# Performance work log

Measured on AMD Instinct MI355X. Metric: run time of the kernel, lower is better.

Reference implementation:

```python
import jax, jax.numpy as jnp
import numpy as np

H = 2048          # hidden_size
NH = 16           # num query heads
NKV = 8           # num kv heads
HD = 128          # head_dim
T = 4096          # tokens (single causal prefill sequence)
THETA = 1000000.0
EPS = 1e-6
QS = NH * HD
KVS = NKV * HD
SCALE = HD ** -0.5


def setup_inputs() -> dict:
    key = jax.random.key(0)
    k0, k1, k2 = jax.random.split(key, 3)
    return {
        "positions": jnp.arange(T, dtype=jnp.int32),
        "hidden_states": jax.random.normal(k0, (T, H), jnp.float32),
        "w_qkv": jax.random.normal(k1, (H, QS + 2 * KVS), jnp.float32) * 0.02,
        "w_o": jax.random.normal(k2, (QS, H), jnp.float32) * 0.02,
        "q_norm_w": jnp.ones((HD,), jnp.float32),
        "k_norm_w": jnp.ones((HD,), jnp.float32),
    }


def _rmsnorm(x, w):
    # per-head RMSNorm over last dim (head_dim)
    return x * jax.lax.rsqrt(jnp.mean(x * x, axis=-1, keepdims=True) + EPS) * w


def _rope(x, cos, sin):
    # neox-style rotate-half RoPE; x: [T, nheads, HD], cos/sin: [T, 1, HD/2]
    x1, x2 = jnp.split(x, 2, axis=-1)
    return jnp.concatenate([x1 * cos - x2 * sin, x2 * cos + x1 * sin], axis=-1)


def reference(positions, hidden_states, w_qkv, w_o, q_norm_w, k_norm_w):
    # fused QKV projection then split
    qkv = hidden_states @ w_qkv                      # [T, QS+2*KVS]
    q, k, v = jnp.split(qkv, [QS, QS + KVS], axis=-1)
    q = _rmsnorm(q.reshape(T, NH, HD), q_norm_w)     # per-head QK RMSNorm
    k = _rmsnorm(k.reshape(T, NKV, HD), k_norm_w)
    v = v.reshape(T, NKV, HD)

    # RoPE over full head_dim
    inv_freq = 1.0 / (THETA ** (jnp.arange(0, HD, 2, dtype=jnp.float32) / HD))
    ang = positions.astype(jnp.float32)[:, None] * inv_freq  # [T, HD/2]
    cos = jnp.cos(ang)[:, None, :]
    sin = jnp.sin(ang)[:, None, :]
    q = _rope(q, cos, sin)
    k = _rope(k, cos, sin)

    # causal GQA attention (prefill path of RadixAttention)
    G = NH // NKV
    q4 = q.reshape(T, NKV, G, HD) * SCALE
    scores = jnp.einsum('tkgd,skd->kgts', q4, k)     # [NKV, G, T, T]
    causal = jnp.tril(jnp.ones((T, T), dtype=bool))
    scores = jnp.where(causal, scores, jnp.float32(-1e30))
    probs = jax.nn.softmax(scores, axis=-1)
    out = jnp.einsum('kgts,skd->tkgd', probs, v).reshape(T, QS)
    return out @ w_o
```

## Files before the change

kernel.cpp:

```cpp
#include <hip/hip_runtime.h>
#include <hip/hip_bf16.h>
#include <math.h>

#define T_TOK 4096
#define H_DIM 2048
#define NH 16
#define NKV 8
#define HD 128
#define QS (NH * HD)
#define KVS (NKV * HD)
#define QKV_W (QS + 2*KVS)
#define QSCALE (0.08838834764831845f * 1.4426950408889634f)
#define EPS 1e-6f

typedef short short8 __attribute__((ext_vector_type(8)));
typedef short short4v __attribute__((ext_vector_type(4)));
typedef float floatx4 __attribute__((ext_vector_type(4)));

#if __has_builtin(__builtin_amdgcn_exp2f)
#define EXP2(x) __builtin_amdgcn_exp2f(x)
#else
#define EXP2(x) exp2f(x)
#endif

__device__ __forceinline__ unsigned short f2bf(float f) {
    unsigned int u = __float_as_uint(f);
    unsigned int r = (u + 0x7FFFu + ((u >> 16) & 1u)) >> 16;
    return (unsigned short)r;
}
__device__ __forceinline__ float bf2f(unsigned short u) {
    unsigned int v = ((unsigned int)u) << 16;
    return __uint_as_float(v);
}
__device__ __forceinline__ unsigned int pk2(float a, float b) {
    union { __hip_bfloat162 h; unsigned int u; } c;
    c.h = __float22bfloat162_rn(make_float2(a, b));
    return c.u;
}

__device__ __forceinline__ void gload_lds16(const unsigned short* g, unsigned short* l) {
    __builtin_amdgcn_global_load_lds(
        (const __attribute__((address_space(1))) unsigned int*)(const void*)g,
        (__attribute__((address_space(3))) unsigned int*)(void*)l, 16, 0, 0);
}

__global__ __launch_bounds__(256) void cvt_bf16(const float* __restrict__ in,
                                                unsigned short* __restrict__ out) {
    int idx = (blockIdx.x * 256 + threadIdx.x) * 8;
    float4 v0 = *(const float4*)&in[idx];
    float4 v1 = *(const float4*)&in[idx + 4];
    short8 t;
    t[0] = (short)f2bf(v0.x); t[1] = (short)f2bf(v0.y);
    t[2] = (short)f2bf(v0.z); t[3] = (short)f2bf(v0.w);
    t[4] = (short)f2bf(v1.x); t[5] = (short)f2bf(v1.y);
    t[6] = (short)f2bf(v1.z); t[7] = (short)f2bf(v1.w);
    *(short8*)&out[idx] = t;
}

__global__ __launch_bounds__(256) void cvt_transpose(const float* __restrict__ in,
                                                     unsigned short* __restrict__ out,
                                                     int K, int N) {
    __shared__ __align__(16) unsigned short t[64][72];
    const int tid = threadIdx.x;
    const int n0 = blockIdx.x * 64, k0 = blockIdx.y * 64;
    const int r = tid >> 4, c4 = (tid & 15) * 4;
    #pragma unroll
    for (int i = 0; i < 4; ++i) {
        int kk = r + 16 * i;
        float4 v = *(const float4*)&in[(size_t)(k0 + kk) * N + n0 + c4];
        t[c4 + 0][kk] = f2bf(v.x); t[c4 + 1][kk] = f2bf(v.y);
        t[c4 + 2][kk] = f2bf(v.z); t[c4 + 3][kk] = f2bf(v.w);
    }
    __syncthreads();
    const int n = tid >> 2, c8 = (tid & 3) * 16;
    short8 a = *(const short8*)&t[n][c8];
    short8 b = *(const short8*)&t[n][c8 + 8];
    *(short8*)&out[(size_t)(n0 + n) * K + k0 + c8] = a;
    *(short8*)&out[(size_t)(n0 + n) * K + k0 + c8 + 8] = b;
}

template<bool C_BF16>
__global__ __launch_bounds__(256) void gemm_bt(const unsigned short* __restrict__ A, int lda,
                                               const unsigned short* __restrict__ Bt, int ldb,
                                               void* __restrict__ Cptr, int ldc, int K) {
    __shared__ __align__(16) unsigned short As[128 * 32];
    __shared__ __align__(16) unsigned short Bs[128 * 32];
    const int tid = threadIdx.x;
    const int wave = tid >> 6, lane = tid & 63;
    const int quad = lane >> 4, l16 = lane & 15;
    const int wm = wave >> 1, wn = wave & 1;
    const int bm = blockIdx.y * 128, bn = blockIdx.x * 128;

    floatx4 acc[4][4] = {};
    for (int k0 = 0; k0 < K; k0 += 32) {
        #pragma unroll
        for (int i = 0; i < 2; ++i) {
            int c = wave * 128 + i * 64 + lane;
            int row = c >> 2, off = (c & 3) * 8;
            gload_lds16(A  + (size_t)(bm + row) * lda + k0 + off, As + (size_t)(wave * 128 + i * 64) * 8);
            gload_lds16(Bt + (size_t)(bn + row) * ldb + k0 + off, Bs + (size_t)(wave * 128 + i * 64) * 8);
        }
        __syncthreads();
        short8 a[4], b[4];
        #pragma unroll
        for (int mi = 0; mi < 4; ++mi)
            a[mi] = *(const short8*)&As[(wm * 64 + mi * 16 + l16) * 32 + quad * 8];
        #pragma unroll
        for (int ni = 0; ni < 4; ++ni)
            b[ni] = *(const short8*)&Bs[(wn * 64 + ni * 16 + l16) * 32 + quad * 8];
        #pragma unroll
        for (int mi = 0; mi < 4; ++mi)
            #pragma unroll
            for (int ni = 0; ni < 4; ++ni)
                acc[mi][ni] = __builtin_amdgcn_mfma_f32_16x16x32_bf16(a[mi], b[ni], acc[mi][ni], 0, 0, 0);
        __syncthreads();
    }
    #pragma unroll
    for (int mi = 0; mi < 4; ++mi)
        #pragma unroll
        for (int ni = 0; ni < 4; ++ni)
            #pragma unroll
            for (int r = 0; r < 4; ++r) {
                int row = bm + wm * 64 + mi * 16 + quad * 4 + r;
                int col = bn + wn * 64 + ni * 16 + l16;
                if (C_BF16)
                    ((unsigned short*)Cptr)[(size_t)row * ldc + col] = f2bf(acc[mi][ni][r]);
                else
                    ((float*)Cptr)[(size_t)row * ldc + col] = acc[mi][ni][r];
            }
}

__global__ __launch_bounds__(256) void rms_rope_bf16(unsigned short* __restrict__ qkv,
                                                     const int* __restrict__ positions,
                                                     const float* __restrict__ qw,
                                                     const float* __restrict__ kw) {
    const int t = blockIdx.x;
    const int wave = threadIdx.x >> 6;
    const int lane = threadIdx.x & 63;
    const float pos = (float)positions[t];
    unsigned short* row = qkv + (size_t)t * QKV_W;
    const float inv_freq = powf(1000000.0f, -(float)lane / 64.0f);
    float sv, cv;
    sincosf(pos * inv_freq, &sv, &cv);
    for (int h = wave; h < NH + NKV; h += 4) {
        unsigned short* x = row + h * HD;
        const float* w = (h < NH) ? qw : kw;
        const float hs = (h < NH) ? QSCALE : 1.0f;
        float x1 = bf2f(x[lane]);
        float x2 = bf2f(x[lane + 64]);
        float ss = x1 * x1 + x2 * x2;
        #pragma unroll
        for (int off = 32; off > 0; off >>= 1) ss += __shfl_xor(ss, off, 64);
        float r = rsqrtf(ss * (1.0f / 128.0f) + EPS) * hs;
        float n1 = x1 * r * w[lane];
        float n2 = x2 * r * w[lane + 64];
        x[lane]      = f2bf(n1 * cv - n2 * sv);
        x[lane + 64] = f2bf(n2 * cv + n1 * sv);
    }
}

__global__ __launch_bounds__(256) void kv_pack(const unsigned short* __restrict__ qkv,
                                               unsigned short* __restrict__ Kp,
                                               unsigned short* __restrict__ Vp) {
    const int tile = blockIdx.x, kvh = blockIdx.y, tid = threadIdx.x;
    const int t0 = tile * 128;
    const size_t tb = (size_t)(kvh * 32 + tile) * 16384;
    #pragma unroll
    for (int i = 0; i < 8; ++i) {
        int cid = i * 256 + tid;
        int s = cid >> 4, c = cid & 15;
        short8 v = *(const short8*)&qkv[(size_t)(t0 + s) * QKV_W + QS + kvh * HD + c * 8];
        *(short8*)&Kp[tb + (s * 16 + (c ^ (s & 7))) * 8] = v;
    }
    __shared__ __align__(16) unsigned short Lt[128 * 136];
    #pragma unroll
    for (int i = 0; i < 8; ++i) {
        int cid = i * 256 + tid;
        int s = cid >> 4, c = cid & 15;
        short8 v = *(const short8*)&qkv[(size_t)(t0 + s) * QKV_W + QS + KVS + kvh * HD + c * 8];
        #pragma unroll
        for (int e = 0; e < 8; ++e)
            Lt[(c * 8 + e) * 136 + s] = (unsigned short)v[e];
    }
    __syncthreads();
    #pragma unroll
    for (int i = 0; i < 8; ++i) {
        int cid = i * 256 + tid;
        int d = cid >> 4, cs = cid & 15;
        short8 v = *(const short8*)&Lt[d * 136 + cs * 8];
        short8 w;
        if ((d >> 3) & 1) {
            #pragma unroll
            for (int e = 0; e < 8; ++e) w[e] = v[e ^ 4];
        } else w = v;
        *(short8*)&Vp[tb + (d * 16 + (cs ^ (d & 7))) * 8] = w;
    }
}

__global__ __launch_bounds__(256, 2) void attn_mfma(unsigned short* __restrict__ qkv,
                                                    const unsigned short* __restrict__ Kp,
                                                    const unsigned short* __restrict__ Vp) {
    __shared__ __align__(16) unsigned short Ks[128 * 128];
    __shared__ __align__(16) unsigned short Vs[128 * 128];
    const int bx = blockIdx.x;
    const int h = bx & 15, kvh = h >> 1;
    const int g = bx >> 4;
    const int qt = (g < 16) ? (31 - g) : (g - 16);
    const int tid = threadIdx.x;
    const int wave = tid >> 6, lane = tid & 63;
    const int quad = lane >> 4, l16 = lane & 15;
    const int t0 = qt * 128;
    const int wrow0 = t0 + wave * 32;
    const int swz = l16 & 7;
    const int hsel = (l16 >> 3) & 1;
    const int vhalf = ((quad & 1) ^ hsel) * 4;
    const int q2 = quad >> 1;

    short8 qf[2][4];
    #pragma unroll
    for (int rt = 0; rt < 2; ++rt)
        #pragma unroll
        for (int ks = 0; ks < 4; ++ks) {
            int rowg = t0 + wave * 32 + rt * 16 + l16;
            qf[rt][ks] = *(const short8*)&qkv[(size_t)rowg * QKV_W + h * HD + ks * 32 + quad * 8];
        }

    float l_s[2] = {};
    floatx4 oacc[2][8] = {};

    for (int st = 0; st <= qt; ++st) {
        const int s0 = st * 128;
        const unsigned short* kb = Kp + (size_t)(kvh * 32 + st) * 16384;
        const unsigned short* vb = Vp + (size_t)(kvh * 32 + st) * 16384;
        #pragma unroll
        for (int i = 0; i < 8; ++i) {
            int ch = i * 256 + tid;
            gload_lds16(kb + (size_t)ch * 8, Ks + (i * 256 + wave * 64) * 8);
        }
        #pragma unroll
        for (int i = 0; i < 8; ++i) {
            int ch = i * 256 + tid;
            gload_lds16(vb + (size_t)ch * 8, Vs + (i * 256 + wave * 64) * 8);
        }
        __syncthreads();

        const bool diag = (st == qt);
        #pragma unroll
        for (int ct = 0; ct < 8; ++ct) {
            const int smin = s0 + ct * 16;
            if (diag && smin > wrow0 + 31) continue;
            floatx4 sacc[2] = {};
            #pragma unroll
            for (int ks = 0; ks < 4; ++ks) {
                short8 kfr = *(const short8*)&Ks[(ct * 16 + l16) * 128 + ((ks * 4 + quad) ^ swz) * 8];
                sacc[0] = __builtin_amdgcn_mfma_f32_16x16x32_bf16(kfr, qf[0][ks], sacc[0], 0, 0, 0);
                sacc[1] = __builtin_amdgcn_mfma_f32_16x16x32_bf16(kfr, qf[1][ks], sacc[1], 0, 0, 0);
            }
            short4v pp[2];
            #pragma unroll
            for (int rt = 0; rt < 2; ++rt) {
                const int tg = wrow0 + rt * 16 + l16;
                float p[4];
                float lsum = 0.0f;
                #pragma unroll
                for (int r = 0; r < 4; ++r) {
                    float s = sacc[rt][r];
                    if (diag && (smin + quad * 4 + r > tg)) s = -1e30f;
                    p[r] = EXP2(s);
                    lsum += p[r];
                }
                l_s[rt] += lsum;
                union { short4v s4; unsigned int u[2]; } pk;
                pk.u[0] = pk2(p[0], p[1]);
                pk.u[1] = pk2(p[2], p[3]);
                pp[rt] = pk.s4;
            }
            const int vc = (((ct * 2 + q2) ^ swz)) * 8 + vhalf;
#if __has_builtin(__builtin_amdgcn_mfma_f32_16x16x16bf16_1k)
            #pragma unroll
            for (int dct = 0; dct < 8; ++dct) {
                short4v bfr = *(const short4v*)&Vs[(dct * 16 + l16) * 128 + vc];
                oacc[0][dct] = __builtin_amdgcn_mfma_f32_16x16x16bf16_1k(pp[0], bfr, oacc[0][dct], 0, 0, 0);
                oacc[1][dct] = __builtin_amdgcn_mfma_f32_16x16x16bf16_1k(pp[1], bfr, oacc[1][dct], 0, 0, 0);
            }
#else
            #pragma unroll
            for (int dct = 0; dct < 8; ++dct) {
                union { short8 s8; short4v s4[2]; } b;
                b.s4[0] = *(const short4v*)&Vs[(dct * 16 + l16) * 128 + vc];
                b.s4[1] = short4v{0, 0, 0, 0};
                #pragma unroll
                for (int rt = 0; rt < 2; ++rt) {
                    union { short8 s8; short4v s4[2]; } a;
                    a.s4[0] = pp[rt];
                    a.s4[1] = short4v{0, 0, 0, 0};
                    oacc[rt][dct] = __builtin_amdgcn_mfma_f32_16x16x32_bf16(a.s8, b.s8, oacc[rt][dct], 0, 0, 0);
                }
            }
#endif
        }
        __syncthreads();
    }

    float lred[2];
    #pragma unroll
    for (int rt = 0; rt < 2; ++rt) {
        float l = l_s[rt];
        l += __shfl_xor(l, 16, 64);
        l += __shfl_xor(l, 32, 64);
        lred[rt] = l;
    }
    #pragma unroll
    for (int rt = 0; rt < 2; ++rt)
        #pragma unroll
        for (int r = 0; r < 4; ++r) {
            float l = __shfl(lred[rt], quad * 4 + r, 64);
            float linv = 1.0f / l;
            int rowg = t0 + wave * 32 + rt * 16 + quad * 4 + r;
            #pragma unroll
            for (int dct = 0; dct < 8; ++dct)
                qkv[(size_t)rowg * QKV_W + h * HD + dct * 16 + l16] = f2bf(oacc[rt][dct][r] * linv);
        }
}

extern "C" void kernel_launch(void* const* d_in, const int* in_sizes, int n_in,
                              void* d_out, int out_size, void* d_ws, size_t ws_size,
                              hipStream_t stream) {
    const int*   positions = (const int*)d_in[0];
    const float* hidden    = (const float*)d_in[1];
    const float* w_qkv     = (const float*)d_in[2];
    const float* w_o       = (const float*)d_in[3];
    const float* q_norm_w  = (const float*)d_in[4];
    const float* k_norm_w  = (const float*)d_in[5];
    float* out = (float*)d_out;

    unsigned short* qkvb   = (unsigned short*)d_ws;
    unsigned short* h_bf   = (unsigned short*)((char*)d_ws + ((size_t)32 << 20));
    unsigned short* Kp     = (unsigned short*)((char*)d_ws + ((size_t)32 << 20));
    unsigned short* Vp     = (unsigned short*)((char*)d_ws + ((size_t)40 << 20));
    unsigned short* wqkv_t = (unsigned short*)((char*)d_ws + ((size_t)48 << 20));
    unsigned short* wo_t   = (unsigned short*)((char*)d_ws + ((size_t)48 << 20));

    cvt_bf16<<<(T_TOK * H_DIM) / (256 * 8), 256, 0, stream>>>(hidden, h_bf);
    cvt_transpose<<<dim3(QKV_W / 64, H_DIM / 64), 256, 0, stream>>>(w_qkv, wqkv_t, H_DIM, QKV_W);
    gemm_bt<true><<<dim3(QKV_W / 128, T_TOK / 128), 256, 0, stream>>>(
        h_bf, H_DIM, wqkv_t, H_DIM, qkvb, QKV_W, H_DIM);
    rms_rope_bf16<<<T_TOK, 256, 0, stream>>>(qkvb, positions, q_norm_w, k_norm_w);
    kv_pack<<<dim3(T_TOK / 128, NKV), 256, 0, stream>>>(qkvb, Kp, Vp);
    cvt_transpose<<<dim3(H_DIM / 64, QS / 64), 256, 0, stream>>>(w_o, wo_t, QS, H_DIM);
    attn_mfma<<<512, 256, 0, stream>>>(qkvb, Kp, Vp);
    gemm_bt<false><<<dim3(H_DIM / 128, T_TOK / 128), 256, 0, stream>>>(
        qkvb, QKV_W, wo_t, QS, out, H_DIM, QS);
}
```

Measured before the change: 410.2 us.

## Replace GEMM with 256x256-tile multistage pipelined kernel using swizzled LDS

Replaces the 128x128 single-buffered bf16 MFMA GEMM with a 256x256-tile, 512-thread kernel. It streams K through a four-slot LDS ring using direct global-to-LDS loads, with manual vmcnt waits and barriers. The kernel also XOR-swizzles LDS columns to reduce bank conflicts, remaps block indices for L2 locality, and raises wave priority around the MFMA bursts. It is meant to hide global-load latency and improve operand reuse in both projection GEMMs. The cost is fewer blocks (256 and 128) on a large-CU device, plus heavier register and LDS use.

```diff
diff --git a/kernel.cpp b/kernel.cpp
--- a/kernel.cpp
+++ b/kernel.cpp
@@ -80,48 +80,103 @@
 }
 
 template<bool C_BF16>
-__global__ __launch_bounds__(256) void gemm_bt(const unsigned short* __restrict__ A, int lda,
-                                               const unsigned short* __restrict__ Bt, int ldb,
-                                               void* __restrict__ Cptr, int ldc, int K) {
-    __shared__ __align__(16) unsigned short As[128 * 32];
-    __shared__ __align__(16) unsigned short Bs[128 * 32];
-    const int tid = threadIdx.x;
+__global__ __launch_bounds__(512, 2) void gemm256(const unsigned short* __restrict__ A, int lda,
+                                                  const unsigned short* __restrict__ Bt, int ldb,
+                                                  void* __restrict__ Cptr, int ldc, int K, int nbx) {
+    __shared__ __align__(16) unsigned short lds[4 * 16384];
+    const int tid  = threadIdx.x;
     const int wave = tid >> 6, lane = tid & 63;
     const int quad = lane >> 4, l16 = lane & 15;
-    const int wm = wave >> 1, wn = wave & 1;
-    const int bm = blockIdx.y * 128, bn = blockIdx.x * 128;
-
-    floatx4 acc[4][4] = {};
-    for (int k0 = 0; k0 < K; k0 += 32) {
-        #pragma unroll
-        for (int i = 0; i < 2; ++i) {
-            int c = wave * 128 + i * 64 + lane;
-            int row = c >> 2, off = (c & 3) * 8;
-            gload_lds16(A  + (size_t)(bm + row) * lda + k0 + off, As + (size_t)(wave * 128 + i * 64) * 8);
-            gload_lds16(Bt + (size_t)(bn + row) * ldb + k0 + off, Bs + (size_t)(wave * 128 + i * 64) * 8);
-        }
-        __syncthreads();
-        short8 a[4], b[4];
-        #pragma unroll
-        for (int mi = 0; mi < 4; ++mi)
-            a[mi] = *(const short8*)&As[(wm * 64 + mi * 16 + l16) * 32 + quad * 8];
+    const int wm = wave >> 2, wn = wave & 3;
+
+    const int cpx = gridDim.x >> 3;
+    const int swz = (blockIdx.x & 7) * cpx + (blockIdx.x >> 3);
+    const int by = swz / nbx, bx = swz % nbx;
+    const int bm = by * 256, bn = bx * 256;
+
+    const int ch0 = wave * 64 + lane;
+    const int ch1 = 512 + ch0;
+    const int ar0 = ch0 >> 2, ac0 = ((ch0 & 3) ^ (ar0 & 3)) * 8;
+    const int ar1 = ch1 >> 2, ac1 = ((ch1 & 3) ^ (ar1 & 3)) * 8;
+    const unsigned short* a0 = A  + (size_t)(bm + ar0) * lda + ac0;
+    const unsigned short* a1 = A  + (size_t)(bm + ar1) * lda + ac1;
+    const unsigned short* b0 = Bt + (size_t)(bn + ar0) * ldb + ac0;
+    const unsigned short* b1 = Bt + (size_t)(bn + ar1) * ldb + ac1;
+    const unsigned du0 = (unsigned)(wave * 64) * 8;
+    const unsigned du1 = (unsigned)(512 + wave * 64) * 8;
+
+    auto stage = [&](int kofs, int sb) {
+        gload_lds16(a0 + kofs, &lds[sb + du0]);
+        gload_lds16(a1 + kofs, &lds[sb + du1]);
+        gload_lds16(b0 + kofs, &lds[sb + 8192 + du0]);
+        gload_lds16(b1 + kofs, &lds[sb + 8192 + du1]);
+    };
+
+    floatx4 acc[8][4] = {};
+    const int arow = wm * 128 + l16;
+    const int brow = wn * 64 + l16;
+    const int sslot = (quad ^ (l16 & 3)) * 8;
+
+    auto compute = [&](int cbo) {
+        short8 bfr[4];
         #pragma unroll
         for (int ni = 0; ni < 4; ++ni)
-            b[ni] = *(const short8*)&Bs[(wn * 64 + ni * 16 + l16) * 32 + quad * 8];
-        #pragma unroll
-        for (int mi = 0; mi < 4; ++mi)
+            bfr[ni] = *(const short8*)&lds[cbo + 8192 + (brow + ni * 16) * 32 + sslot];
+        __builtin_amdgcn_s_setprio(1);
+        #pragma unroll
+        for (int mi = 0; mi < 8; ++mi) {
+            short8 afr = *(const short8*)&lds[cbo + (arow + mi * 16) * 32 + sslot];
             #pragma unroll
             for (int ni = 0; ni < 4; ++ni)
-                acc[mi][ni] = __builtin_amdgcn_mfma_f32_16x16x32_bf16(a[mi], b[ni], acc[mi][ni], 0, 0, 0);
-        __syncthreads();
-    }
-    #pragma unroll
-    for (int mi = 0; mi < 4; ++mi)
+                acc[mi][ni] = __builtin_amdgcn_mfma_f32_16x16x32_bf16(afr, bfr[ni], acc[mi][ni], 0, 0, 0);
+        }
+        __builtin_amdgcn_s_setprio(0);
+    };
+
+    const int NT = K >> 5;
+    stage(0,  0);
+    stage(32, 16384);
+    stage(64, 32768);
+
+    int cb = 0;
+    for (int t = 0; t < NT - 3; ++t) {
+        stage((t + 3) * 32, (cb + 3 * 16384) & 65535);
+        asm volatile("s_waitcnt vmcnt(12)" ::: "memory");
+        __builtin_amdgcn_s_barrier();
+        asm volatile("" ::: "memory");
+        compute(cb);
+        asm volatile("" ::: "memory");
+        __builtin_amdgcn_s_barrier();
+        cb = (cb + 16384) & 65535;
+    }
+    asm volatile("s_waitcnt vmcnt(8)" ::: "memory");
+    __builtin_amdgcn_s_barrier();
+    asm volatile("" ::: "memory");
+    compute(cb);
+    asm volatile("" ::: "memory");
+    __builtin_amdgcn_s_barrier();
+    cb = (cb + 16384) & 65535;
+
+    asm volatile("s_waitcnt vmcnt(4)" ::: "memory");
+    __builtin_amdgcn_s_barrier();
+    asm volatile("" ::: "memory");
+    compute(cb);
+    asm volatile("" ::: "memory");
+    __builtin_amdgcn_s_barrier();
+    cb = (cb + 16384) & 65535;
+
+    asm volatile("s_waitcnt vmcnt(0)" ::: "memory");
+    __builtin_amdgcn_s_barrier();
+    asm volatile("" ::: "memory");
+    compute(cb);
+
+    #pragma unroll
+    for (int mi = 0; mi < 8; ++mi)
         #pragma unroll
         for (int ni = 0; ni < 4; ++ni)
             #pragma unroll
             for (int r = 0; r < 4; ++r) {
-                int row = bm + wm * 64 + mi * 16 + quad * 4 + r;
+                int row = bm + wm * 128 + mi * 16 + quad * 4 + r;
                 int col = bn + wn * 64 + ni * 16 + l16;
                 if (C_BF16)
                     ((unsigned short*)Cptr)[(size_t)row * ldc + col] = f2bf(acc[mi][ni][r]);
@@ -343,12 +398,12 @@
 
     cvt_bf16<<<(T_TOK * H_DIM) / (256 * 8), 256, 0, stream>>>(hidden, h_bf);
     cvt_transpose<<<dim3(QKV_W / 64, H_DIM / 64), 256, 0, stream>>>(w_qkv, wqkv_t, H_DIM, QKV_W);
-    gemm_bt<true><<<dim3(QKV_W / 128, T_TOK / 128), 256, 0, stream>>>(
-        h_bf, H_DIM, wqkv_t, H_DIM, qkvb, QKV_W, H_DIM);
+    gemm256<true><<<dim3(256), 512, 0, stream>>>(
+        h_bf, H_DIM, wqkv_t, H_DIM, qkvb, QKV_W, H_DIM, QKV_W / 256);
     rms_rope_bf16<<<T_TOK, 256, 0, stream>>>(qkvb, positions, q_norm_w, k_norm_w);
     kv_pack<<<dim3(T_TOK / 128, NKV), 256, 0, stream>>>(qkvb, Kp, Vp);
     cvt_transpose<<<dim3(H_DIM / 64, QS / 64), 256, 0, stream>>>(w_o, wo_t, QS, H_DIM);
     attn_mfma<<<512, 256, 0, stream>>>(qkvb, Kp, Vp);
-    gemm_bt<false><<<dim3(H_DIM / 128, T_TOK / 128), 256, 0, stream>>>(
-        qkvb, QKV_W, wo_t, QS, out, H_DIM, QS);
-}
+    gemm256<false><<<dim3(128), 512, 0, stream>>>(
+        qkvb, QKV_W, wo_t, QS, out, H_DIM, QS, H_DIM / 256);
+}
```

After: 384.5 us. 6.2% less time.

## Add 8-wave 256x256 pipelined GEMM for QKV projection with XCD-aware block swizzle

Applied to the files above, without the earlier changes.

Adds a new 512-thread GEMM kernel that uses 256x256 output tiles, double-buffered direct-to-LDS global loads staged in quarters, and interleaves LDS fragment reads with MFMA groups under barriers and priority bumps. The QKV projection now uses it, with blocks remapped so neighbouring tiles land on the same XCD. The change also replaces powf with exp2f for the RoPE frequencies and rotates the V transpose LDS write order to reduce bank conflicts. The aim is better MFMA utilisation and overlap of memory with compute in the largest GEMM, at the cost of high register pressure (128 accumulators per lane) and a fixed grid of 256 blocks.

```diff
diff --git a/kernel.cpp b/kernel.cpp
--- a/kernel.cpp
+++ b/kernel.cpp
@@ -130,6 +130,116 @@
             }
 }
 
+template<bool C_BF16>
+__global__ __launch_bounds__(512, 2) void gemm8p(const unsigned short* __restrict__ A, int lda,
+                                                 const unsigned short* __restrict__ Bt, int ldb,
+                                                 void* __restrict__ Cptr, int ldc, int K, int nbx) {
+    __shared__ __align__(16) unsigned short lds[2 * 32768];
+    const int tid  = threadIdx.x;
+    const int wave = tid >> 6, lane = tid & 63;
+    const int quad = lane >> 4, l16 = lane & 15;
+    const int wm = wave >> 2, wn = wave & 3;
+
+    const int cpx = gridDim.x >> 3;
+    const int swzb = (blockIdx.x & 7) * cpx + (blockIdx.x >> 3);
+    const int by = swzb / nbx, bx = swzb % nbx;
+    const int bm = by * 256, bn = bx * 256;
+
+    const int ch0 = wave * 64 + lane, ch1 = 512 + ch0;
+    const int r0 = ch0 >> 3, gc0 = ((ch0 & 7) ^ (r0 & 7)) * 8;
+    const int r1 = ch1 >> 3, gc1 = ((ch1 & 7) ^ (r1 & 7)) * 8;
+    const unsigned du0 = (unsigned)(wave * 64) * 8;
+    const unsigned du1 = (unsigned)(512 + wave * 64) * 8;
+
+    auto stage = [&](int kt, int hf, int buf) {
+        const int panel = hf & 1, rhalf = (hf >> 1) * 128;
+        const unsigned short* P = panel ? Bt : A;
+        const int bp = panel ? bn : bm;
+        const int ld = panel ? ldb : lda;
+        unsigned short* dst = &lds[buf * 32768 + panel * 16384 + rhalf * 64];
+        gload_lds16(P + (size_t)(bp + rhalf + r0) * ld + kt * 64 + gc0, dst + du0);
+        gload_lds16(P + (size_t)(bp + rhalf + r1) * ld + kt * 64 + gc1, dst + du1);
+    };
+
+    floatx4 acc[8][4] = {};
+    const int arowb = wm * 128 + l16;
+    const int browb = wn * 64 + l16;
+    const int sw = l16 & 7;
+
+    short8 bfr[4], afr[4];
+    auto rdB = [&](int cur, int kk) {
+        const int sl = ((kk * 4 + quad) ^ sw) * 8;
+        #pragma unroll
+        for (int ni = 0; ni < 4; ++ni)
+            bfr[ni] = *(const short8*)&lds[cur * 32768 + 16384 + (browb + ni * 16) * 64 + sl];
+    };
+    auto rdA = [&](int cur, int mh, int kk) {
+        const int sl = ((kk * 4 + quad) ^ sw) * 8;
+        #pragma unroll
+        for (int mi = 0; mi < 4; ++mi)
+            afr[mi] = *(const short8*)&lds[cur * 32768 + (arowb + (mh * 4 + mi) * 16) * 64 + sl];
+    };
+    auto mfma16 = [&](int mh) {
+        asm volatile("s_waitcnt lgkmcnt(0)" ::: "memory");
+        __builtin_amdgcn_s_setprio(1);
+        #pragma unroll
+        for (int mi = 0; mi < 4; ++mi)
+            #pragma unroll
+            for (int ni = 0; ni < 4; ++ni)
+                acc[mh * 4 + mi][ni] =
+                    __builtin_amdgcn_mfma_f32_16x16x32_bf16(afr[mi], bfr[ni], acc[mh * 4 + mi][ni], 0, 0, 0);
+        __builtin_amdgcn_s_setprio(0);
+    };
+
+    const int NT = K >> 6;
+    stage(0, 0, 0); stage(0, 1, 0); stage(0, 2, 0); stage(0, 3, 0);
+
+    int cur = 0;
+    for (int kt = 0; kt < NT; ++kt) {
+        const bool last = (kt == NT - 1);
+        if (!last) {
+            stage(kt + 1, 0, cur ^ 1);
+            asm volatile("s_waitcnt vmcnt(2)" ::: "memory");
+        } else {
+            asm volatile("s_waitcnt vmcnt(0)" ::: "memory");
+        }
+        __builtin_amdgcn_s_barrier();
+        rdB(cur, 0); rdA(cur, 0, 0);
+        mfma16(0);
+        __builtin_amdgcn_s_barrier();
+        rdA(cur, 1, 0);
+        if (!last) stage(kt + 1, 1, cur ^ 1);
+        __builtin_amdgcn_s_barrier();
+        mfma16(1);
+        __builtin_amdgcn_s_barrier();
+        rdB(cur, 1); rdA(cur, 0, 1);
+        if (!last) stage(kt + 1, 2, cur ^ 1);
+        __builtin_amdgcn_s_barrier();
+        mfma16(0);
+        __builtin_amdgcn_s_barrier();
+        rdA(cur, 1, 1);
+        if (!last) stage(kt + 1, 3, cur ^ 1);
+        __builtin_amdgcn_s_barrier();
+        mfma16(1);
+        __builtin_amdgcn_s_barrier();
+        cur ^= 1;
+    }
+
+    #pragma unroll
+    for (int mi = 0; mi < 8; ++mi)
+        #pragma unroll
+        for (int ni = 0; ni < 4; ++ni)
+            #pragma unroll
+            for (int r = 0; r < 4; ++r) {
+                int row = bm + wm * 128 + mi * 16 + quad * 4 + r;
+                int col = bn + wn * 64 + ni * 16 + l16;
+                if (C_BF16)
+                    ((unsigned short*)Cptr)[(size_t)row * ldc + col] = f2bf(acc[mi][ni][r]);
+                else
+                    ((float*)Cptr)[(size_t)row * ldc + col] = acc[mi][ni][r];
+            }
+}
+
 __global__ __launch_bounds__(256) void rms_rope_bf16(unsigned short* __restrict__ qkv,
                                                      const int* __restrict__ positions,
                                                      const float* __restrict__ qw,
@@ -139,7 +249,7 @@
     const int lane = threadIdx.x & 63;
     const float pos = (float)positions[t];
     unsigned short* row = qkv + (size_t)t * QKV_W;
-    const float inv_freq = powf(1000000.0f, -(float)lane / 64.0f);
+    const float inv_freq = exp2f(-(float)lane * (19.931568569324174f / 64.0f));
     float sv, cv;
     sincosf(pos * inv_freq, &sv, &cv);
     for (int h = wave; h < NH + NKV; h += 4) {
@@ -179,8 +289,10 @@
         int s = cid >> 4, c = cid & 15;
         short8 v = *(const short8*)&qkv[(size_t)(t0 + s) * QKV_W + QS + KVS + kvh * HD + c * 8];
         #pragma unroll
-        for (int e = 0; e < 8; ++e)
-            Lt[(c * 8 + e) * 136 + s] = (unsigned short)v[e];
+        for (int e = 0; e < 8; ++e) {
+            int ee = (e + c) & 7;
+            Lt[(c * 8 + ee) * 136 + s] = (unsigned short)v[ee];
+        }
     }
     __syncthreads();
     #pragma unroll
@@ -343,8 +455,8 @@
 
     cvt_bf16<<<(T_TOK * H_DIM) / (256 * 8), 256, 0, stream>>>(hidden, h_bf);
     cvt_transpose<<<dim3(QKV_W / 64, H_DIM / 64), 256, 0, stream>>>(w_qkv, wqkv_t, H_DIM, QKV_W);
-    gemm_bt<true><<<dim3(QKV_W / 128, T_TOK / 128), 256, 0, stream>>>(
-        h_bf, H_DIM, wqkv_t, H_DIM, qkvb, QKV_W, H_DIM);
+    gemm8p<true><<<dim3(256), 512, 0, stream>>>(
+        h_bf, H_DIM, wqkv_t, H_DIM, qkvb, QKV_W, H_DIM, QKV_W / 256);
     rms_rope_bf16<<<T_TOK, 256, 0, stream>>>(qkvb, positions, q_norm_w, k_norm_w);
     kv_pack<<<dim3(T_TOK / 128, NKV), 256, 0, stream>>>(qkvb, Kp, Vp);
     cvt_transpose<<<dim3(H_DIM / 64, QS / 64), 256, 0, stream>>>(w_o, wo_t, QS, H_DIM);
```

Measured after the change: 369.6 us. 1.11x faster.

## Replace GEMM with double-buffered 256-row tile kernel using swizzled LDS and block remap

Applied to the files above, without the earlier changes.

Replaces the 128x128 single-buffered bf16 GEMM with a 512-thread kernel that uses 256xBN tiles and a K-step of 64. It double-buffers LDS with direct global-to-LDS loads, XOR-swizzles columns to avoid bank conflicts, and remaps block IDs for better L2 locality. It also raises MFMA priority during compute. Smaller tweaks replace powf with exp2f for the RoPE frequencies and rotate the write order in the V transpose to reduce LDS bank conflicts. The larger tiles raise register and LDS pressure per block, which can lower occupancy.

```diff
diff --git a/kernel.cpp b/kernel.cpp
--- a/kernel.cpp
+++ b/kernel.cpp
@@ -79,50 +79,96 @@
     *(short8*)&out[(size_t)(n0 + n) * K + k0 + c8 + 8] = b;
 }
 
-template<bool C_BF16>
-__global__ __launch_bounds__(256) void gemm_bt(const unsigned short* __restrict__ A, int lda,
-                                               const unsigned short* __restrict__ Bt, int ldb,
-                                               void* __restrict__ Cptr, int ldc, int K) {
-    __shared__ __align__(16) unsigned short As[128 * 32];
-    __shared__ __align__(16) unsigned short Bs[128 * 32];
-    const int tid = threadIdx.x;
+template<bool C_BF16, int BN>
+__global__ __launch_bounds__(512, 2) void gemm8p(const unsigned short* __restrict__ A, int lda,
+                                                 const unsigned short* __restrict__ Bt, int ldb,
+                                                 void* __restrict__ Cptr, int ldc, int K, int nbx) {
+    constexpr int LDSTILE = 16384 + BN * 64;
+    constexpr int NFRAG = BN / 64;
+    __shared__ __align__(16) unsigned short lds[2 * LDSTILE];
+    const int tid  = threadIdx.x;
     const int wave = tid >> 6, lane = tid & 63;
     const int quad = lane >> 4, l16 = lane & 15;
-    const int wm = wave >> 1, wn = wave & 1;
-    const int bm = blockIdx.y * 128, bn = blockIdx.x * 128;
-
-    floatx4 acc[4][4] = {};
-    for (int k0 = 0; k0 < K; k0 += 32) {
-        #pragma unroll
-        for (int i = 0; i < 2; ++i) {
-            int c = wave * 128 + i * 64 + lane;
-            int row = c >> 2, off = (c & 3) * 8;
-            gload_lds16(A  + (size_t)(bm + row) * lda + k0 + off, As + (size_t)(wave * 128 + i * 64) * 8);
-            gload_lds16(Bt + (size_t)(bn + row) * ldb + k0 + off, Bs + (size_t)(wave * 128 + i * 64) * 8);
-        }
-        __syncthreads();
-        short8 a[4], b[4];
-        #pragma unroll
-        for (int mi = 0; mi < 4; ++mi)
-            a[mi] = *(const short8*)&As[(wm * 64 + mi * 16 + l16) * 32 + quad * 8];
-        #pragma unroll
-        for (int ni = 0; ni < 4; ++ni)
-            b[ni] = *(const short8*)&Bs[(wn * 64 + ni * 16 + l16) * 32 + quad * 8];
-        #pragma unroll
-        for (int mi = 0; mi < 4; ++mi)
-            #pragma unroll
-            for (int ni = 0; ni < 4; ++ni)
-                acc[mi][ni] = __builtin_amdgcn_mfma_f32_16x16x32_bf16(a[mi], b[ni], acc[mi][ni], 0, 0, 0);
-        __syncthreads();
-    }
-    #pragma unroll
-    for (int mi = 0; mi < 4; ++mi)
-        #pragma unroll
-        for (int ni = 0; ni < 4; ++ni)
+    const int wm = wave >> 2, wn = wave & 3;
+
+    const int cpx = gridDim.x >> 3;
+    const int swzb = (blockIdx.x & 7) * cpx + (blockIdx.x >> 3);
+    const int by = swzb / nbx, bx = swzb % nbx;
+    const int bm = by * 256, bn = bx * BN;
+
+    const int ch0 = wave * 64 + lane, ch1 = 512 + ch0;
+    const int r0 = ch0 >> 3, gc0 = ((ch0 & 7) ^ (r0 & 7)) * 8;
+    const int r1 = ch1 >> 3, gc1 = ((ch1 & 7) ^ (r1 & 7)) * 8;
+    const unsigned du0 = (unsigned)(wave * 64) * 8;
+    const unsigned du1 = (unsigned)(512 + wave * 64) * 8;
+
+    auto stageP = [&](const unsigned short* P, int bp, int ld,
+                      unsigned short* dstbase, int rhalf, int kt) {
+        unsigned short* dst = dstbase + rhalf * 64;
+        gload_lds16(P + (size_t)(bp + rhalf + r0) * ld + kt * 64 + gc0, dst + du0);
+        gload_lds16(P + (size_t)(bp + rhalf + r1) * ld + kt * 64 + gc1, dst + du1);
+    };
+    auto stage = [&](int kt, int buf) {
+        unsigned short* ab = &lds[buf * LDSTILE];
+        unsigned short* bb = ab + 16384;
+        stageP(A, bm, lda, ab, 0, kt);
+        stageP(A, bm, lda, ab, 128, kt);
+        stageP(Bt, bn, ldb, bb, 0, kt);
+        if (BN == 256) stageP(Bt, bn, ldb, bb, 128, kt);
+    };
+
+    floatx4 acc[8][NFRAG] = {};
+    const int arowb = wm * 128 + l16;
+    const int browb = wn * (BN / 4) + l16;
+    const int sw = l16 & 7;
+
+    auto compute = [&](int buf) {
+        const unsigned short* ab = &lds[buf * LDSTILE];
+        const unsigned short* bb = ab + 16384;
+        __builtin_amdgcn_s_setprio(1);
+        #pragma unroll
+        for (int kk = 0; kk < 2; ++kk) {
+            const int sl = ((kk * 4 + quad) ^ sw) * 8;
+            short8 bfr[NFRAG];
+            #pragma unroll
+            for (int ni = 0; ni < NFRAG; ++ni)
+                bfr[ni] = *(const short8*)&bb[(browb + ni * 16) * 64 + sl];
+            #pragma unroll
+            for (int mh = 0; mh < 2; ++mh) {
+                short8 afr[4];
+                #pragma unroll
+                for (int mi = 0; mi < 4; ++mi)
+                    afr[mi] = *(const short8*)&ab[(arowb + (mh * 4 + mi) * 16) * 64 + sl];
+                #pragma unroll
+                for (int mi = 0; mi < 4; ++mi)
+                    #pragma unroll
+                    for (int ni = 0; ni < NFRAG; ++ni)
+                        acc[mh * 4 + mi][ni] =
+                            __builtin_amdgcn_mfma_f32_16x16x32_bf16(afr[mi], bfr[ni], acc[mh * 4 + mi][ni], 0, 0, 0);
+            }
+        }
+        __builtin_amdgcn_s_setprio(0);
+    };
+
+    const int NT = K >> 6;
+    stage(0, 0);
+    int cur = 0;
+    for (int kt = 0; kt < NT; ++kt) {
+        asm volatile("s_waitcnt vmcnt(0)" ::: "memory");
+        __builtin_amdgcn_s_barrier();
+        if (kt + 1 < NT) stage(kt + 1, cur ^ 1);
+        compute(cur);
+        cur ^= 1;
+    }
+
+    #pragma unroll
+    for (int mi = 0; mi < 8; ++mi)
+        #pragma unroll
+        for (int ni = 0; ni < NFRAG; ++ni)
             #pragma unroll
             for (int r = 0; r < 4; ++r) {
-                int row = bm + wm * 64 + mi * 16 + quad * 4 + r;
-                int col = bn + wn * 64 + ni * 16 + l16;
+                int row = bm + wm * 128 + mi * 16 + quad * 4 + r;
+                int col = bn + wn * (BN / 4) + ni * 16 + l16;
                 if (C_BF16)
                     ((unsigned short*)Cptr)[(size_t)row * ldc + col] = f2bf(acc[mi][ni][r]);
                 else
@@ -139,7 +185,7 @@
     const int lane = threadIdx.x & 63;
     const float pos = (float)positions[t];
     unsigned short* row = qkv + (size_t)t * QKV_W;
-    const float inv_freq = powf(1000000.0f, -(float)lane / 64.0f);
+    const float inv_freq = exp2f(-(float)lane * (19.931568569324174f / 64.0f));
     float sv, cv;
     sincosf(pos * inv_freq, &sv, &cv);
     for (int h = wave; h < NH + NKV; h += 4) {
@@ -179,8 +225,10 @@
         int s = cid >> 4, c = cid & 15;
         short8 v = *(const short8*)&qkv[(size_t)(t0 + s) * QKV_W + QS + KVS + kvh * HD + c * 8];
         #pragma unroll
-        for (int e = 0; e < 8; ++e)
-            Lt[(c * 8 + e) * 136 + s] = (unsigned short)v[e];
+        for (int e = 0; e < 8; ++e) {
+            int ee = (e + c) & 7;
+            Lt[(c * 8 + ee) * 136 + s] = (unsigned short)v[ee];
+        }
     }
     __syncthreads();
     #pragma unroll
@@ -343,12 +391,12 @@
 
     cvt_bf16<<<(T_TOK * H_DIM) / (256 * 8), 256, 0, stream>>>(hidden, h_bf);
     cvt_transpose<<<dim3(QKV_W / 64, H_DIM / 64), 256, 0, stream>>>(w_qkv, wqkv_t, H_DIM, QKV_W);
-    gemm_bt<true><<<dim3(QKV_W / 128, T_TOK / 128), 256, 0, stream>>>(
-        h_bf, H_DIM, wqkv_t, H_DIM, qkvb, QKV_W, H_DIM);
+    gemm8p<true, 256><<<dim3(256), 512, 0, stream>>>(
+        h_bf, H_DIM, wqkv_t, H_DIM, qkvb, QKV_W, H_DIM, QKV_W / 256);
     rms_rope_bf16<<<T_TOK, 256, 0, stream>>>(qkvb, positions, q_norm_w, k_norm_w);
     kv_pack<<<dim3(T_TOK / 128, NKV), 256, 0, stream>>>(qkvb, Kp, Vp);
     cvt_transpose<<<dim3(H_DIM / 64, QS / 64), 256, 0, stream>>>(w_o, wo_t, QS, H_DIM);
     attn_mfma<<<512, 256, 0, stream>>>(qkvb, Kp, Vp);
-    gemm_bt<false><<<dim3(H_DIM / 128, T_TOK / 128), 256, 0, stream>>>(
-        qkvb, QKV_W, wo_t, QS, out, H_DIM, QS);
-}
+    gemm8p<false, 128><<<dim3(256), 512, 0, stream>>>(
+        qkvb, QKV_W, wo_t, QS, out, H_DIM, QS, H_DIM / 128);
+}
```

After: 344.8 us. 1.19x faster.
